# Performance work log

Hardware: AMD Instinct MI355X
Metric: run time of the kernel (lower is better)

Reference implementation:

```python
import jax, jax.numpy as jnp
import numpy as np

DIM = 1024
DEPTH = 7
PAR = 8
N_NODES = 2 ** (DEPTH + 1) - 1  # 255
WIDTH = PAR * N_NODES  # 2040


def setup_inputs() -> dict:
    key = jax.random.key(0)
    k1, k2, k3, k4 = jax.random.split(key, 4)
    init_k = float(np.sqrt(1.0 / DIM))
    init_k2 = float(np.sqrt(1.0 / ((DEPTH + 1) * PAR)))
    oldx = jax.random.normal(k1, (4, 2048, DIM), dtype=jnp.float32)
    W_in = jax.random.uniform(k2, (WIDTH, DIM), jnp.float32, -init_k, init_k)
    b_in = jax.random.uniform(k3, (WIDTH,), jnp.float32, -init_k, init_k)
    W_out = jax.random.uniform(k4, (DIM, WIDTH), jnp.float32, -init_k2, init_k2)
    return {"oldx": oldx, "W_in": W_in, "b_in": b_in, "W_out": W_out}


def reference(oldx, W_in, b_in, W_out):
    x = oldx.reshape(-1, DIM)                      # [B, dim]
    B = x.shape[0]
    logits = x @ W_in.T + b_in                     # [B, width] dense GEMM over ALL nodes
    decisions = (logits > 0).astype(jnp.int32).reshape(B, PAR, N_NODES)
    acts = jax.nn.silu(logits).reshape(B, PAR, N_NODES)

    # Tree traversal: mark root, then descend DEPTH levels by each node's sign bit.
    current = jnp.zeros((B, PAR), dtype=jnp.int32)
    dmap = jax.nn.one_hot(current, N_NODES, dtype=acts.dtype)  # root node marked
    for d in range(DEPTH):
        cur_platform = 2 ** d - 1
        next_platform = 2 ** (d + 1) - 1
        moves = jnp.take_along_axis(decisions, current[..., None], axis=2)[..., 0]
        current = (current - cur_platform) * 2 + moves + next_platform
        dmap = dmap + jax.nn.one_hot(current, N_NODES, dtype=acts.dtype)

    masked = acts * jax.lax.stop_gradient(dmap)    # only depth+1 nodes per tree survive
    out = masked.reshape(B, WIDTH) @ W_out.T       # [B, dim]
    return out.reshape(oldx.shape)
```

## Files before the change

kernel.cpp:

```cpp
#include <hip/hip_runtime.h>
#include <math.h>

#define DIM 1024
#define DEPTH 7
#define PAR 8
#define N_NODES 255
#define WIDTH 2040
#define MARGIN 0.03f

#define REPLANE(p) ((((p) & 1) << 3) | ((((p) >> 1) & 1) << 4) | ((((p) >> 2) & 1) << 5))

typedef float  float2v  __attribute__((ext_vector_type(2)));
typedef _Float16 half2v __attribute__((ext_vector_type(2)));

__device__ __forceinline__ unsigned short f32_to_bf16(float f) {
    unsigned int u = __float_as_uint(f);
    u += 0x7fffu + ((u >> 16) & 1u);
    return (unsigned short)(u >> 16);
}
__device__ __forceinline__ float bf_lo(unsigned int u) { return __uint_as_float(u << 16); }
__device__ __forceinline__ float bf_hi(unsigned int u) { return __uint_as_float(u & 0xffff0000u); }

__device__ __forceinline__ half2v as_h2(unsigned int u) {
    union { unsigned int u; half2v h; } c; c.u = u; return c.h;
}
__device__ __forceinline__ unsigned int pack_h2(float a, float b) {
    union { half2v h; unsigned int u; } c;
    c.h = (half2v){(_Float16)a, (_Float16)b};
    return c.u;
}

__device__ __forceinline__ float dot2h(unsigned int a, unsigned int b, float c) {
#if __has_builtin(__builtin_amdgcn_fdot2)
    return __builtin_amdgcn_fdot2(as_h2(a), as_h2(b), c, false);
#else
    half2v ha = as_h2(a), hb = as_h2(b);
    c = fmaf((float)ha.x, (float)hb.x, c);
    return fmaf((float)ha.y, (float)hb.y, c);
#endif
}

__device__ __forceinline__ float foldK(float a, float b, int K) {
    const bool hi = (threadIdx.x & (unsigned)K) != 0;
    const float keep = hi ? b : a;
    const float send = hi ? a : b;
    return keep + __shfl_xor(send, K, 64);
}

__global__ __launch_bounds__(256) void convert_f16_kernel(
    const float* __restrict__ src, unsigned int* __restrict__ dst, int n4)
{
    int i = (int)(blockIdx.x * blockDim.x + threadIdx.x);
    if (i < n4) {
        float4 v = ((const float4*)src)[i];
        uint2 pk;
        pk.x = pack_h2(v.x, v.y);
        pk.y = pack_h2(v.z, v.w);
        ((uint2*)dst)[i] = pk;
    }
}

__global__ __launch_bounds__(256) void transpose_bf16_kernel(
    const float* __restrict__ W_out, unsigned short* __restrict__ WoT)
{
    __shared__ float tile[64][65];
    const int w0 = blockIdx.x * 64;
    const int d0 = blockIdx.y * 64;
    const int tid = (int)threadIdx.x;
    const int sub = tid & 15;
    const int grp = tid >> 4;

    #pragma unroll
    for (int pass = 0; pass < 4; ++pass) {
        const int dl = pass * 16 + grp;
        const int wl = sub * 4;
        const int w = w0 + wl;
        const int d = d0 + dl;
        float4 v = make_float4(0.f, 0.f, 0.f, 0.f);
        if (w + 3 < WIDTH) {
            v = *(const float4*)(W_out + (size_t)d * WIDTH + w);
        } else {
            float t0 = (w + 0 < WIDTH) ? W_out[(size_t)d * WIDTH + w + 0] : 0.f;
            float t1 = (w + 1 < WIDTH) ? W_out[(size_t)d * WIDTH + w + 1] : 0.f;
            float t2 = (w + 2 < WIDTH) ? W_out[(size_t)d * WIDTH + w + 2] : 0.f;
            float t3 = (w + 3 < WIDTH) ? W_out[(size_t)d * WIDTH + w + 3] : 0.f;
            v = make_float4(t0, t1, t2, t3);
        }
        tile[dl][wl + 0] = v.x; tile[dl][wl + 1] = v.y;
        tile[dl][wl + 2] = v.z; tile[dl][wl + 3] = v.w;
    }
    __syncthreads();
    #pragma unroll
    for (int pass = 0; pass < 4; ++pass) {
        const int wl = pass * 16 + grp;
        const int dl = sub * 4;
        const int w = w0 + wl;
        if (w < WIDTH) {
            unsigned int b0 = f32_to_bf16(tile[dl + 0][wl]);
            unsigned int b1 = f32_to_bf16(tile[dl + 1][wl]);
            unsigned int b2 = f32_to_bf16(tile[dl + 2][wl]);
            unsigned int b3 = f32_to_bf16(tile[dl + 3][wl]);
            uint2 pk;
            pk.x = b0 | (b1 << 16);
            pk.y = b2 | (b3 << 16);
            *(uint2*)(WoT + (size_t)w * DIM + d0 + dl) = pk;
        }
    }
}

__global__ __launch_bounds__(256, 2) void fff_f16_kernel(
    const float* __restrict__ x,
    const float* __restrict__ W_in,
    const float* __restrict__ b_in,
    const unsigned int* __restrict__ Wh,
    const unsigned short* __restrict__ WoT,
    float* __restrict__ out,
    int B)
{
    const int wave = (int)((blockIdx.x * blockDim.x + threadIdx.x) >> 6);
    const int lane = (int)(threadIdx.x & 63);
    if (wave >= B) return;

    const float* xr = x + (size_t)wave * DIM;
    unsigned int xp[8];
    {
        float4 a0 = *(const float4*)(xr + lane * 8 + 0);
        float4 a1 = *(const float4*)(xr + lane * 8 + 4);
        float4 a2 = *(const float4*)(xr + 512 + lane * 8 + 0);
        float4 a3 = *(const float4*)(xr + 512 + lane * 8 + 4);
        xp[0] = pack_h2(a0.x, a0.y);
        xp[1] = pack_h2(a0.z, a0.w);
        xp[2] = pack_h2(a1.x, a1.y);
        xp[3] = pack_h2(a1.z, a1.w);
        xp[4] = pack_h2(a2.x, a2.y);
        xp[5] = pack_h2(a2.z, a2.w);
        xp[6] = pack_h2(a3.x, a3.y);
        xp[7] = pack_h2(a3.z, a3.w);
    }

    float2v acc2[8];
    #pragma unroll
    for (int i = 0; i < 8; ++i) acc2[i] = (float2v){0.f, 0.f};

    unsigned long long nodes = 0ULL;
    const int myp = ((lane >> 3) & 1) | (((lane >> 4) & 1) << 1) | (((lane >> 5) & 1) << 2);

    #pragma unroll 1
    for (int d = 0; d <= DEPTH; ++d) {
        int gidx[PAR];
        float partial[PAR];
        uint4 wo0[PAR], wo1[PAR];

        #pragma unroll
        for (int p = 0; p < PAR; ++p) {
            const int np = (int)((nodes >> (8 * p)) & 0xffULL);
            gidx[p] = p * N_NODES + np;
        }
        #pragma unroll
        for (int p = 0; p < PAR; ++p) {
            const unsigned short* wo = WoT + (size_t)gidx[p] * DIM;
            wo0[p] = *(const uint4*)(wo + lane * 8);
            wo1[p] = *(const uint4*)(wo + 512 + lane * 8);
        }
        #pragma unroll
        for (int p = 0; p < PAR; ++p) {
            const unsigned int* wr = Wh + (size_t)gidx[p] * (DIM / 2);
            const uint4 u0 = *(const uint4*)(wr + lane * 4);
            const uint4 u1 = *(const uint4*)(wr + 256 + lane * 4);
            float s = 0.f;
            s = dot2h(xp[0], u0.x, s);
            s = dot2h(xp[1], u0.y, s);
            s = dot2h(xp[2], u0.z, s);
            s = dot2h(xp[3], u0.w, s);
            s = dot2h(xp[4], u1.x, s);
            s = dot2h(xp[5], u1.y, s);
            s = dot2h(xp[6], u1.z, s);
            s = dot2h(xp[7], u1.w, s);
            partial[p] = s;
        }

        const float c01 = foldK(partial[0], partial[1], 8);
        const float c23 = foldK(partial[2], partial[3], 8);
        const float c45 = foldK(partial[4], partial[5], 8);
        const float c67 = foldK(partial[6], partial[7], 8);
        const float d0f = foldK(c01, c23, 16);
        const float d1f = foldK(c45, c67, 16);
        float e = foldK(d0f, d1f, 32);
        e += __shfl_xor(e, 1, 64);
        e += __shfl_xor(e, 2, 64);
        e += __shfl_xor(e, 4, 64);

        const int ga = (lane & 8) ? gidx[1] : gidx[0];
        const int gb = (lane & 8) ? gidx[3] : gidx[2];
        const int gc = (lane & 8) ? gidx[5] : gidx[4];
        const int gd = (lane & 8) ? gidx[7] : gidx[6];
        const int ge = (lane & 16) ? gb : ga;
        const int gf = (lane & 16) ? gd : gc;
        const int gmine = (lane & 32) ? gf : ge;
        float my = e + b_in[gmine];

        if (d < DEPTH) {
            const unsigned long long bal = __ballot(fabsf(my) < MARGIN);
            unsigned rm = 0;
            #pragma unroll
            for (int p = 0; p < PAR; ++p)
                rm |= ((unsigned)((bal >> REPLANE(p)) & 1ULL)) << p;
            if (rm) {
                const float4 fa = *(const float4*)(xr + lane * 8 + 0);
                const float4 fb = *(const float4*)(xr + lane * 8 + 4);
                const float4 fc = *(const float4*)(xr + 512 + lane * 8 + 0);
                const float4 fd = *(const float4*)(xr + 512 + lane * 8 + 4);
                while (rm) {
                    const int p = __builtin_ctz(rm); rm &= (rm - 1u);
                    const int np = (int)((nodes >> (8 * p)) & 0xffULL);
                    const int gi = p * N_NODES + np;
                    const float* wr = W_in + (size_t)gi * DIM;
                    const float4 wa = *(const float4*)(wr + lane * 8 + 0);
                    const float4 wb = *(const float4*)(wr + lane * 8 + 4);
                    const float4 wc = *(const float4*)(wr + 512 + lane * 8 + 0);
                    const float4 wd = *(const float4*)(wr + 512 + lane * 8 + 4);
                    float s = 0.f;
                    s = fmaf(fa.x, wa.x, s); s = fmaf(fa.y, wa.y, s);
                    s = fmaf(fa.z, wa.z, s); s = fmaf(fa.w, wa.w, s);
                    s = fmaf(fb.x, wb.x, s); s = fmaf(fb.y, wb.y, s);
                    s = fmaf(fb.z, wb.z, s); s = fmaf(fb.w, wb.w, s);
                    s = fmaf(fc.x, wc.x, s); s = fmaf(fc.y, wc.y, s);
                    s = fmaf(fc.z, wc.z, s); s = fmaf(fc.w, wc.w, s);
                    s = fmaf(fd.x, wd.x, s); s = fmaf(fd.y, wd.y, s);
                    s = fmaf(fd.z, wd.z, s); s = fmaf(fd.w, wd.w, s);
                    #pragma unroll
                    for (int off = 32; off >= 1; off >>= 1)
                        s += __shfl_xor(s, off, 64);
                    const float lf = s + b_in[gi];
                    my = (myp == p) ? lf : my;
                }
            }
        }

        const float act_mine = my / (1.0f + __expf(-my));
        const unsigned long long pos = __ballot(my > 0.0f);

        float act[PAR];
        #pragma unroll
        for (int p = 0; p < PAR; ++p)
            act[p] = __shfl(act_mine, REPLANE(p), 64);

        #pragma unroll
        for (int p = 0; p < PAR; ++p) {
            const uint4 u0 = wo0[p];
            const uint4 u1 = wo1[p];
            const float2v a2 = (float2v){act[p], act[p]};
            acc2[0] += a2 * (float2v){bf_lo(u0.x), bf_hi(u0.x)};
            acc2[1] += a2 * (float2v){bf_lo(u0.y), bf_hi(u0.y)};
            acc2[2] += a2 * (float2v){bf_lo(u0.z), bf_hi(u0.z)};
            acc2[3] += a2 * (float2v){bf_lo(u0.w), bf_hi(u0.w)};
            acc2[4] += a2 * (float2v){bf_lo(u1.x), bf_hi(u1.x)};
            acc2[5] += a2 * (float2v){bf_lo(u1.y), bf_hi(u1.y)};
            acc2[6] += a2 * (float2v){bf_lo(u1.z), bf_hi(u1.z)};
            acc2[7] += a2 * (float2v){bf_lo(u1.w), bf_hi(u1.w)};

            if (d < DEPTH) {
                const int np = (int)((nodes >> (8 * p)) & 0xffULL);
                const unsigned long long nn = (unsigned long long)
                    (2 * np + 1 + (int)((pos >> REPLANE(p)) & 1ULL));
                nodes = (nodes & ~(0xffULL << (8 * p))) | (nn << (8 * p));
            }
        }
    }

    float* orow = out + (size_t)wave * DIM;
    *(float4*)(orow + lane * 8 + 0) =
        make_float4(acc2[0].x, acc2[0].y, acc2[1].x, acc2[1].y);
    *(float4*)(orow + lane * 8 + 4) =
        make_float4(acc2[2].x, acc2[2].y, acc2[3].x, acc2[3].y);
    *(float4*)(orow + 512 + lane * 8 + 0) =
        make_float4(acc2[4].x, acc2[4].y, acc2[5].x, acc2[5].y);
    *(float4*)(orow + 512 + lane * 8 + 4) =
        make_float4(acc2[6].x, acc2[6].y, acc2[7].x, acc2[7].y);
}

__global__ __launch_bounds__(256) void fff_fallback_kernel(
    const float* __restrict__ x, const float* __restrict__ W_in,
    const float* __restrict__ b_in, const float* __restrict__ W_out,
    float* __restrict__ out, int B)
{
    const int wave = (int)((blockIdx.x * blockDim.x + threadIdx.x) >> 6);
    const int lane = (int)(threadIdx.x & 63);
    if (wave >= B) return;

    const float* xr = x + (size_t)wave * DIM;
    float4 x4[4];
    x4[0] = *(const float4*)(xr + lane * 8 + 0);
    x4[1] = *(const float4*)(xr + lane * 8 + 4);
    x4[2] = *(const float4*)(xr + 512 + lane * 8 + 0);
    x4[3] = *(const float4*)(xr + 512 + lane * 8 + 4);

    float acc[16];
    #pragma unroll
    for (int i = 0; i < 16; ++i) acc[i] = 0.f;
    int node[PAR];
    #pragma unroll
    for (int p = 0; p < PAR; ++p) node[p] = 0;

    for (int d = 0; d <= DEPTH; ++d) {
        #pragma unroll
        for (int p = 0; p < PAR; ++p) {
            const int gidx = p * N_NODES + node[p];
            const float* wr = W_in + (size_t)gidx * DIM;
            const float4 wa = *(const float4*)(wr + lane * 8 + 0);
            const float4 wb = *(const float4*)(wr + lane * 8 + 4);
            const float4 wc = *(const float4*)(wr + 512 + lane * 8 + 0);
            const float4 wd = *(const float4*)(wr + 512 + lane * 8 + 4);
            float s = 0.f;
            s = fmaf(x4[0].x, wa.x, s); s = fmaf(x4[0].y, wa.y, s);
            s = fmaf(x4[0].z, wa.z, s); s = fmaf(x4[0].w, wa.w, s);
            s = fmaf(x4[1].x, wb.x, s); s = fmaf(x4[1].y, wb.y, s);
            s = fmaf(x4[1].z, wb.z, s); s = fmaf(x4[1].w, wb.w, s);
            s = fmaf(x4[2].x, wc.x, s); s = fmaf(x4[2].y, wc.y, s);
            s = fmaf(x4[2].z, wc.z, s); s = fmaf(x4[2].w, wc.w, s);
            s = fmaf(x4[3].x, wd.x, s); s = fmaf(x4[3].y, wd.y, s);
            s = fmaf(x4[3].z, wd.z, s); s = fmaf(x4[3].w, wd.w, s);
            #pragma unroll
            for (int off = 32; off >= 1; off >>= 1)
                s += __shfl_xor(s, off, 64);
            const float logit = s + b_in[gidx];
            const float act = logit / (1.0f + __expf(-logit));
            #pragma unroll
            for (int k = 0; k < 2; ++k) {
                #pragma unroll
                for (int j = 0; j < 8; ++j) {
                    const int e = k * 512 + lane * 8 + j;
                    acc[k * 8 + j] = fmaf(act, W_out[(size_t)e * WIDTH + gidx], acc[k * 8 + j]);
                }
            }
            node[p] = 2 * node[p] + 1 + ((logit > 0.0f) ? 1 : 0);
        }
    }

    float* orow = out + (size_t)wave * DIM;
    *(float4*)(orow + lane * 8 + 0)       = make_float4(acc[0],  acc[1],  acc[2],  acc[3]);
    *(float4*)(orow + lane * 8 + 4)       = make_float4(acc[4],  acc[5],  acc[6],  acc[7]);
    *(float4*)(orow + 512 + lane * 8 + 0) = make_float4(acc[8],  acc[9],  acc[10], acc[11]);
    *(float4*)(orow + 512 + lane * 8 + 4) = make_float4(acc[12], acc[13], acc[14], acc[15]);
}

extern "C" void kernel_launch(void* const* d_in, const int* in_sizes, int n_in,
                              void* d_out, int out_size, void* d_ws, size_t ws_size,
                              hipStream_t stream) {
    const float* oldx  = (const float*)d_in[0];
    const float* W_in  = (const float*)d_in[1];
    const float* b_in  = (const float*)d_in[2];
    const float* W_out = (const float*)d_in[3];
    float* out = (float*)d_out;

    const int B = in_sizes[0] / DIM;

    const size_t half = (size_t)WIDTH * DIM * sizeof(unsigned short);
    const bool use_lp = (ws_size >= 2 * half) && (d_ws != nullptr);

    const int blocks = (B + 3) / 4;

    if (use_lp) {
        unsigned short* WoT = (unsigned short*)d_ws;
        unsigned int*   Wh  = (unsigned int*)((char*)d_ws + half);
        dim3 tg((WIDTH + 63) / 64, DIM / 64);
        transpose_bf16_kernel<<<tg, 256, 0, stream>>>(W_out, WoT);
        const int n4 = WIDTH * DIM / 4;
        convert_f16_kernel<<<(n4 + 255) / 256, 256, 0, stream>>>(W_in, Wh, n4);
        fff_f16_kernel<<<blocks, 256, 0, stream>>>(oldx, W_in, b_in, Wh, WoT, out, B);
    } else {
        fff_fallback_kernel<<<blocks, 256, 0, stream>>>(oldx, W_in, b_in, W_out, out, B);
    }
}
```

Measured before the change: 188.7 us.

## Process two rows per wavefront and defer W_out loads until after activation

Each wavefront now handles two batch rows at once, interleaving their gather loads, dot products, reductions and accumulations so that more independent memory requests are in flight per wave. The W_out row loads move from before the logit computation to just before the accumulation, which shortens register live ranges. The launch-bounds occupancy hint is dropped and the grid is halved. Register pressure roughly doubles, which may reduce occupancy or cause spills, and the rows within a wave can diverge on the rare fp32 recompute path.

```diff
diff --git a/kernel.cpp b/kernel.cpp
--- a/kernel.cpp
+++ b/kernel.cpp
@@ -108,7 +108,7 @@
     }
 }
 
-__global__ __launch_bounds__(256, 2) void fff_f16_kernel(
+__global__ __launch_bounds__(256) void fff_f16x2_kernel(
     const float* __restrict__ x,
     const float* __restrict__ W_in,
     const float* __restrict__ b_in,
@@ -117,166 +117,216 @@
     float* __restrict__ out,
     int B)
 {
-    const int wave = (int)((blockIdx.x * blockDim.x + threadIdx.x) >> 6);
-    const int lane = (int)(threadIdx.x & 63);
-    if (wave >= B) return;
-
-    const float* xr = x + (size_t)wave * DIM;
-    unsigned int xp[8];
+    const int wpair = (int)((blockIdx.x * blockDim.x + threadIdx.x) >> 6);
+    const int lane  = (int)(threadIdx.x & 63);
+    const int r0 = 2 * wpair;
+    const int r1 = 2 * wpair + 1;
+    if (r0 >= B) return;
+    const bool has1 = (r1 < B);
+
+    const float* xr0 = x + (size_t)r0 * DIM;
+    const float* xr1 = x + (size_t)(has1 ? r1 : r0) * DIM;
+
+    unsigned int xp0[8], xp1[8];
     {
-        float4 a0 = *(const float4*)(xr + lane * 8 + 0);
-        float4 a1 = *(const float4*)(xr + lane * 8 + 4);
-        float4 a2 = *(const float4*)(xr + 512 + lane * 8 + 0);
-        float4 a3 = *(const float4*)(xr + 512 + lane * 8 + 4);
-        xp[0] = pack_h2(a0.x, a0.y);
-        xp[1] = pack_h2(a0.z, a0.w);
-        xp[2] = pack_h2(a1.x, a1.y);
-        xp[3] = pack_h2(a1.z, a1.w);
-        xp[4] = pack_h2(a2.x, a2.y);
-        xp[5] = pack_h2(a2.z, a2.w);
-        xp[6] = pack_h2(a3.x, a3.y);
-        xp[7] = pack_h2(a3.z, a3.w);
-    }
-
-    float2v acc2[8];
+        float4 a0 = *(const float4*)(xr0 + lane * 8 + 0);
+        float4 a1 = *(const float4*)(xr0 + lane * 8 + 4);
+        float4 a2 = *(const float4*)(xr0 + 512 + lane * 8 + 0);
+        float4 a3 = *(const float4*)(xr0 + 512 + lane * 8 + 4);
+        float4 b0 = *(const float4*)(xr1 + lane * 8 + 0);
+        float4 b1 = *(const float4*)(xr1 + lane * 8 + 4);
+        float4 b2 = *(const float4*)(xr1 + 512 + lane * 8 + 0);
+        float4 b3 = *(const float4*)(xr1 + 512 + lane * 8 + 4);
+        xp0[0] = pack_h2(a0.x, a0.y); xp0[1] = pack_h2(a0.z, a0.w);
+        xp0[2] = pack_h2(a1.x, a1.y); xp0[3] = pack_h2(a1.z, a1.w);
+        xp0[4] = pack_h2(a2.x, a2.y); xp0[5] = pack_h2(a2.z, a2.w);
+        xp0[6] = pack_h2(a3.x, a3.y); xp0[7] = pack_h2(a3.z, a3.w);
+        xp1[0] = pack_h2(b0.x, b0.y); xp1[1] = pack_h2(b0.z, b0.w);
+        xp1[2] = pack_h2(b1.x, b1.y); xp1[3] = pack_h2(b1.z, b1.w);
+        xp1[4] = pack_h2(b2.x, b2.y); xp1[5] = pack_h2(b2.z, b2.w);
+        xp1[6] = pack_h2(b3.x, b3.y); xp1[7] = pack_h2(b3.z, b3.w);
+    }
+
+    float2v acc0[8], acc1[8];
     #pragma unroll
-    for (int i = 0; i < 8; ++i) acc2[i] = (float2v){0.f, 0.f};
-
-    unsigned long long nodes = 0ULL;
+    for (int i = 0; i < 8; ++i) { acc0[i] = (float2v){0.f, 0.f}; acc1[i] = (float2v){0.f, 0.f}; }
+
+    unsigned long long nodes0 = 0ULL, nodes1 = 0ULL;
     const int myp = ((lane >> 3) & 1) | (((lane >> 4) & 1) << 1) | (((lane >> 5) & 1) << 2);
 
     #pragma unroll 1
     for (int d = 0; d <= DEPTH; ++d) {
-        int gidx[PAR];
-        float partial[PAR];
-        uint4 wo0[PAR], wo1[PAR];
+        int g0[PAR], g1[PAR];
+        float pa0[PAR], pa1[PAR];
 
         #pragma unroll
         for (int p = 0; p < PAR; ++p) {
-            const int np = (int)((nodes >> (8 * p)) & 0xffULL);
-            gidx[p] = p * N_NODES + np;
-        }
+            g0[p] = p * N_NODES + (int)((nodes0 >> (8 * p)) & 0xffULL);
+            g1[p] = p * N_NODES + (int)((nodes1 >> (8 * p)) & 0xffULL);
+        }
+
         #pragma unroll
         for (int p = 0; p < PAR; ++p) {
-            const unsigned short* wo = WoT + (size_t)gidx[p] * DIM;
-            wo0[p] = *(const uint4*)(wo + lane * 8);
-            wo1[p] = *(const uint4*)(wo + 512 + lane * 8);
-        }
+            const unsigned int* wr0 = Wh + (size_t)g0[p] * (DIM / 2);
+            const unsigned int* wr1 = Wh + (size_t)g1[p] * (DIM / 2);
+            const uint4 u0 = *(const uint4*)(wr0 + lane * 4);
+            const uint4 u1 = *(const uint4*)(wr0 + 256 + lane * 4);
+            const uint4 v0 = *(const uint4*)(wr1 + lane * 4);
+            const uint4 v1 = *(const uint4*)(wr1 + 256 + lane * 4);
+            float s0 = 0.f, s1 = 0.f;
+            s0 = dot2h(xp0[0], u0.x, s0);  s1 = dot2h(xp1[0], v0.x, s1);
+            s0 = dot2h(xp0[1], u0.y, s0);  s1 = dot2h(xp1[1], v0.y, s1);
+            s0 = dot2h(xp0[2], u0.z, s0);  s1 = dot2h(xp1[2], v0.z, s1);
+            s0 = dot2h(xp0[3], u0.w, s0);  s1 = dot2h(xp1[3], v0.w, s1);
+            s0 = dot2h(xp0[4], u1.x, s0);  s1 = dot2h(xp1[4], v1.x, s1);
+            s0 = dot2h(xp0[5], u1.y, s0);  s1 = dot2h(xp1[5], v1.y, s1);
+            s0 = dot2h(xp0[6], u1.z, s0);  s1 = dot2h(xp1[6], v1.z, s1);
+            s0 = dot2h(xp0[7], u1.w, s0);  s1 = dot2h(xp1[7], v1.w, s1);
+            pa0[p] = s0; pa1[p] = s1;
+        }
+
+        const float c01a = foldK(pa0[0], pa0[1], 8),  c01b = foldK(pa1[0], pa1[1], 8);
+        const float c23a = foldK(pa0[2], pa0[3], 8),  c23b = foldK(pa1[2], pa1[3], 8);
+        const float c45a = foldK(pa0[4], pa0[5], 8),  c45b = foldK(pa1[4], pa1[5], 8);
+        const float c67a = foldK(pa0[6], pa0[7], 8),  c67b = foldK(pa1[6], pa1[7], 8);
+        const float d0a = foldK(c01a, c23a, 16),      d0b = foldK(c01b, c23b, 16);
+        const float d1a = foldK(c45a, c67a, 16),      d1b = foldK(c45b, c67b, 16);
+        float e0 = foldK(d0a, d1a, 32);
+        float e1 = foldK(d0b, d1b, 32);
+        e0 += __shfl_xor(e0, 1, 64);  e1 += __shfl_xor(e1, 1, 64);
+        e0 += __shfl_xor(e0, 2, 64);  e1 += __shfl_xor(e1, 2, 64);
+        e0 += __shfl_xor(e0, 4, 64);  e1 += __shfl_xor(e1, 4, 64);
+
+        int gm0, gm1;
+        {
+            const int a0 = (lane & 8) ? g0[1] : g0[0];
+            const int a1 = (lane & 8) ? g0[3] : g0[2];
+            const int a2 = (lane & 8) ? g0[5] : g0[4];
+            const int a3 = (lane & 8) ? g0[7] : g0[6];
+            const int b0 = (lane & 16) ? a1 : a0;
+            const int b1 = (lane & 16) ? a3 : a2;
+            gm0 = (lane & 32) ? b1 : b0;
+            const int c0 = (lane & 8) ? g1[1] : g1[0];
+            const int c1 = (lane & 8) ? g1[3] : g1[2];
+            const int c2 = (lane & 8) ? g1[5] : g1[4];
+            const int c3 = (lane & 8) ? g1[7] : g1[6];
+            const int e0i = (lane & 16) ? c1 : c0;
+            const int e1i = (lane & 16) ? c3 : c2;
+            gm1 = (lane & 32) ? e1i : e0i;
+        }
+        float my0 = e0 + b_in[gm0];
+        float my1 = e1 + b_in[gm1];
+
+        if (d < DEPTH) {
+            const unsigned long long bal0 = __ballot(fabsf(my0) < MARGIN);
+            const unsigned long long bal1 = has1 ? __ballot(fabsf(my1) < MARGIN) : 0ULL;
+            unsigned rm0 = 0, rm1 = 0;
+            #pragma unroll
+            for (int p = 0; p < PAR; ++p) {
+                rm0 |= ((unsigned)((bal0 >> REPLANE(p)) & 1ULL)) << p;
+                rm1 |= ((unsigned)((bal1 >> REPLANE(p)) & 1ULL)) << p;
+            }
+            if (rm0 | rm1) {
+                #pragma unroll 1
+                for (int r = 0; r < 2; ++r) {
+                    unsigned rm = r ? rm1 : rm0;
+                    if (!rm) continue;
+                    const float* xrr = r ? xr1 : xr0;
+                    const float4 fa = *(const float4*)(xrr + lane * 8 + 0);
+                    const float4 fb = *(const float4*)(xrr + lane * 8 + 4);
+                    const float4 fc = *(const float4*)(xrr + 512 + lane * 8 + 0);
+                    const float4 fd = *(const float4*)(xrr + 512 + lane * 8 + 4);
+                    while (rm) {
+                        const int p = __builtin_ctz(rm); rm &= (rm - 1u);
+                        const int gi = r ? g1[p] : g0[p];
+                        const float* wr = W_in + (size_t)gi * DIM;
+                        const float4 wa = *(const float4*)(wr + lane * 8 + 0);
+                        const float4 wb = *(const float4*)(wr + lane * 8 + 4);
+                        const float4 wc = *(const float4*)(wr + 512 + lane * 8 + 0);
+                        const float4 wd = *(const float4*)(wr + 512 + lane * 8 + 4);
+                        float s = 0.f;
+                        s = fmaf(fa.x, wa.x, s); s = fmaf(fa.y, wa.y, s);
+                        s = fmaf(fa.z, wa.z, s); s = fmaf(fa.w, wa.w, s);
+                        s = fmaf(fb.x, wb.x, s); s = fmaf(fb.y, wb.y, s);
+                        s = fmaf(fb.z, wb.z, s); s = fmaf(fb.w, wb.w, s);
+                        s = fmaf(fc.x, wc.x, s); s = fmaf(fc.y, wc.y, s);
+                        s = fmaf(fc.z, wc.z, s); s = fmaf(fc.w, wc.w, s);
+                        s = fmaf(fd.x, wd.x, s); s = fmaf(fd.y, wd.y, s);
+                        s = fmaf(fd.z, wd.z, s); s = fmaf(fd.w, wd.w, s);
+                        #pragma unroll
+                        for (int off = 32; off >= 1; off >>= 1)
+                            s += __shfl_xor(s, off, 64);
+                        const float lf = s + b_in[gi];
+                        if (myp == p) { if (r) my1 = lf; else my0 = lf; }
+                    }
+                }
+            }
+        }
+
+        const float am0 = my0 / (1.0f + __expf(-my0));
+        const float am1 = my1 / (1.0f + __expf(-my1));
+        const unsigned long long pos0 = __ballot(my0 > 0.0f);
+        const unsigned long long pos1 = __ballot(my1 > 0.0f);
+
+        float act0[PAR], act1[PAR];
         #pragma unroll
         for (int p = 0; p < PAR; ++p) {
-            const unsigned int* wr = Wh + (size_t)gidx[p] * (DIM / 2);
-            const uint4 u0 = *(const uint4*)(wr + lane * 4);
-            const uint4 u1 = *(const uint4*)(wr + 256 + lane * 4);
-            float s = 0.f;
-            s = dot2h(xp[0], u0.x, s);
-            s = dot2h(xp[1], u0.y, s);
-            s = dot2h(xp[2], u0.z, s);
-            s = dot2h(xp[3], u0.w, s);
-            s = dot2h(xp[4], u1.x, s);
-            s = dot2h(xp[5], u1.y, s);
-            s = dot2h(xp[6], u1.z, s);
-            s = dot2h(xp[7], u1.w, s);
-            partial[p] = s;
-        }
-
-        const float c01 = foldK(partial[0], partial[1], 8);
-        const float c23 = foldK(partial[2], partial[3], 8);
-        const float c45 = foldK(partial[4], partial[5], 8);
-        const float c67 = foldK(partial[6], partial[7], 8);
-        const float d0f = foldK(c01, c23, 16);
-        const float d1f = foldK(c45, c67, 16);
-        float e = foldK(d0f, d1f, 32);
-        e += __shfl_xor(e, 1, 64);
-        e += __shfl_xor(e, 2, 64);
-        e += __shfl_xor(e, 4, 64);
-
-        const int ga = (lane & 8) ? gidx[1] : gidx[0];
-        const int gb = (lane & 8) ? gidx[3] : gidx[2];
-        const int gc = (lane & 8) ? gidx[5] : gidx[4];
-        const int gd = (lane & 8) ? gidx[7] : gidx[6];
-        const int ge = (lane & 16) ? gb : ga;
-        const int gf = (lane & 16) ? gd : gc;
-        const int gmine = (lane & 32) ? gf : ge;
-        float my = e + b_in[gmine];
-
-        if (d < DEPTH) {
-            const unsigned long long bal = __ballot(fabsf(my) < MARGIN);
-            unsigned rm = 0;
-            #pragma unroll
-            for (int p = 0; p < PAR; ++p)
-                rm |= ((unsigned)((bal >> REPLANE(p)) & 1ULL)) << p;
-            if (rm) {
-                const float4 fa = *(const float4*)(xr + lane * 8 + 0);
-                const float4 fb = *(const float4*)(xr + lane * 8 + 4);
-                const float4 fc = *(const float4*)(xr + 512 + lane * 8 + 0);
-                const float4 fd = *(const float4*)(xr + 512 + lane * 8 + 4);
-                while (rm) {
-                    const int p = __builtin_ctz(rm); rm &= (rm - 1u);
-                    const int np = (int)((nodes >> (8 * p)) & 0xffULL);
-                    const int gi = p * N_NODES + np;
-                    const float* wr = W_in + (size_t)gi * DIM;
-                    const float4 wa = *(const float4*)(wr + lane * 8 + 0);
-                    const float4 wb = *(const float4*)(wr + lane * 8 + 4);
-                    const float4 wc = *(const float4*)(wr + 512 + lane * 8 + 0);
-                    const float4 wd = *(const float4*)(wr + 512 + lane * 8 + 4);
-                    float s = 0.f;
-                    s = fmaf(fa.x, wa.x, s); s = fmaf(fa.y, wa.y, s);
-                    s = fmaf(fa.z, wa.z, s); s = fmaf(fa.w, wa.w, s);
-                    s = fmaf(fb.x, wb.x, s); s = fmaf(fb.y, wb.y, s);
-                    s = fmaf(fb.z, wb.z, s); s = fmaf(fb.w, wb.w, s);
-                    s = fmaf(fc.x, wc.x, s); s = fmaf(fc.y, wc.y, s);
-                    s = fmaf(fc.z, wc.z, s); s = fmaf(fc.w, wc.w, s);
-                    s = fmaf(fd.x, wd.x, s); s = fmaf(fd.y, wd.y, s);
-                    s = fmaf(fd.z, wd.z, s); s = fmaf(fd.w, wd.w, s);
-                    #pragma unroll
-                    for (int off = 32; off >= 1; off >>= 1)
-                        s += __shfl_xor(s, off, 64);
-                    const float lf = s + b_in[gi];
-                    my = (myp == p) ? lf : my;
-                }
-            }
-        }
-
-        const float act_mine = my / (1.0f + __expf(-my));
-        const unsigned long long pos = __ballot(my > 0.0f);
-
-        float act[PAR];
-        #pragma unroll
-        for (int p = 0; p < PAR; ++p)
-            act[p] = __shfl(act_mine, REPLANE(p), 64);
+            act0[p] = __shfl(am0, REPLANE(p), 64);
+            act1[p] = __shfl(am1, REPLANE(p), 64);
+        }
 
         #pragma unroll
         for (int p = 0; p < PAR; ++p) {
-            const uint4 u0 = wo0[p];
-            const uint4 u1 = wo1[p];
-            const float2v a2 = (float2v){act[p], act[p]};
-            acc2[0] += a2 * (float2v){bf_lo(u0.x), bf_hi(u0.x)};
-            acc2[1] += a2 * (float2v){bf_lo(u0.y), bf_hi(u0.y)};
-            acc2[2] += a2 * (float2v){bf_lo(u0.z), bf_hi(u0.z)};
-            acc2[3] += a2 * (float2v){bf_lo(u0.w), bf_hi(u0.w)};
-            acc2[4] += a2 * (float2v){bf_lo(u1.x), bf_hi(u1.x)};
-            acc2[5] += a2 * (float2v){bf_lo(u1.y), bf_hi(u1.y)};
-            acc2[6] += a2 * (float2v){bf_lo(u1.z), bf_hi(u1.z)};
-            acc2[7] += a2 * (float2v){bf_lo(u1.w), bf_hi(u1.w)};
+            const unsigned short* wo0 = WoT + (size_t)g0[p] * DIM;
+            const unsigned short* wo1 = WoT + (size_t)g1[p] * DIM;
+            const uint4 u0 = *(const uint4*)(wo0 + lane * 8);
+            const uint4 u1 = *(const uint4*)(wo0 + 512 + lane * 8);
+            const uint4 v0 = *(const uint4*)(wo1 + lane * 8);
+            const uint4 v1 = *(const uint4*)(wo1 + 512 + lane * 8);
+            const float2v A0 = (float2v){act0[p], act0[p]};
+            const float2v A1 = (float2v){act1[p], act1[p]};
+            acc0[0] += A0 * (float2v){bf_lo(u0.x), bf_hi(u0.x)};
+            acc0[1] += A0 * (float2v){bf_lo(u0.y), bf_hi(u0.y)};
+            acc0[2] += A0 * (float2v){bf_lo(u0.z), bf_hi(u0.z)};
+            acc0[3] += A0 * (float2v){bf_lo(u0.w), bf_hi(u0.w)};
+            acc0[4] += A0 * (float2v){bf_lo(u1.x), bf_hi(u1.x)};
+            acc0[5] += A0 * (float2v){bf_lo(u1.y), bf_hi(u1.y)};
+            acc0[6] += A0 * (float2v){bf_lo(u1.z), bf_hi(u1.z)};
+            acc0[7] += A0 * (float2v){bf_lo(u1.w), bf_hi(u1.w)};
+            acc1[0] += A1 * (float2v){bf_lo(v0.x), bf_hi(v0.x)};
+            acc1[1] += A1 * (float2v){bf_lo(v0.y), bf_hi(v0.y)};
+            acc1[2] += A1 * (float2v){bf_lo(v0.z), bf_hi(v0.z)};
+            acc1[3] += A1 * (float2v){bf_lo(v0.w), bf_hi(v0.w)};
+            acc1[4] += A1 * (float2v){bf_lo(v1.x), bf_hi(v1.x)};
+            acc1[5] += A1 * (float2v){bf_lo(v1.y), bf_hi(v1.y)};
+            acc1[6] += A1 * (float2v){bf_lo(v1.z), bf_hi(v1.z)};
+            acc1[7] += A1 * (float2v){bf_lo(v1.w), bf_hi(v1.w)};
 
             if (d < DEPTH) {
-                const int np = (int)((nodes >> (8 * p)) & 0xffULL);
-                const unsigned long long nn = (unsigned long long)
-                    (2 * np + 1 + (int)((pos >> REPLANE(p)) & 1ULL));
-                nodes = (nodes & ~(0xffULL << (8 * p))) | (nn << (8 * p));
+                const int np0 = (int)((nodes0 >> (8 * p)) & 0xffULL);
+                const int np1 = (int)((nodes1 >> (8 * p)) & 0xffULL);
+                const unsigned long long nn0 = (unsigned long long)
+                    (2 * np0 + 1 + (int)((pos0 >> REPLANE(p)) & 1ULL));
+                const unsigned long long nn1 = (unsigned long long)
+                    (2 * np1 + 1 + (int)((pos1 >> REPLANE(p)) & 1ULL));
+                nodes0 = (nodes0 & ~(0xffULL << (8 * p))) | (nn0 << (8 * p));
+                nodes1 = (nodes1 & ~(0xffULL << (8 * p))) | (nn1 << (8 * p));
             }
         }
     }
 
-    float* orow = out + (size_t)wave * DIM;
-    *(float4*)(orow + lane * 8 + 0) =
-        make_float4(acc2[0].x, acc2[0].y, acc2[1].x, acc2[1].y);
-    *(float4*)(orow + lane * 8 + 4) =
-        make_float4(acc2[2].x, acc2[2].y, acc2[3].x, acc2[3].y);
-    *(float4*)(orow + 512 + lane * 8 + 0) =
-        make_float4(acc2[4].x, acc2[4].y, acc2[5].x, acc2[5].y);
-    *(float4*)(orow + 512 + lane * 8 + 4) =
-        make_float4(acc2[6].x, acc2[6].y, acc2[7].x, acc2[7].y);
+    float* o0 = out + (size_t)r0 * DIM;
+    *(float4*)(o0 + lane * 8 + 0)       = make_float4(acc0[0].x, acc0[0].y, acc0[1].x, acc0[1].y);
+    *(float4*)(o0 + lane * 8 + 4)       = make_float4(acc0[2].x, acc0[2].y, acc0[3].x, acc0[3].y);
+    *(float4*)(o0 + 512 + lane * 8 + 0) = make_float4(acc0[4].x, acc0[4].y, acc0[5].x, acc0[5].y);
+    *(float4*)(o0 + 512 + lane * 8 + 4) = make_float4(acc0[6].x, acc0[6].y, acc0[7].x, acc0[7].y);
+    if (has1) {
+        float* o1 = out + (size_t)r1 * DIM;
+        *(float4*)(o1 + lane * 8 + 0)       = make_float4(acc1[0].x, acc1[0].y, acc1[1].x, acc1[1].y);
+        *(float4*)(o1 + lane * 8 + 4)       = make_float4(acc1[2].x, acc1[2].y, acc1[3].x, acc1[3].y);
+        *(float4*)(o1 + 512 + lane * 8 + 0) = make_float4(acc1[4].x, acc1[4].y, acc1[5].x, acc1[5].y);
+        *(float4*)(o1 + 512 + lane * 8 + 4) = make_float4(acc1[6].x, acc1[6].y, acc1[7].x, acc1[7].y);
+    }
 }
 
 __global__ __launch_bounds__(256) void fff_fallback_kernel(
@@ -358,8 +408,6 @@
     const size_t half = (size_t)WIDTH * DIM * sizeof(unsigned short);
     const bool use_lp = (ws_size >= 2 * half) && (d_ws != nullptr);
 
-    const int blocks = (B + 3) / 4;
-
     if (use_lp) {
         unsigned short* WoT = (unsigned short*)d_ws;
         unsigned int*   Wh  = (unsigned int*)((char*)d_ws + half);
@@ -367,8 +415,11 @@
         transpose_bf16_kernel<<<tg, 256, 0, stream>>>(W_out, WoT);
         const int n4 = WIDTH * DIM / 4;
         convert_f16_kernel<<<(n4 + 255) / 256, 256, 0, stream>>>(W_in, Wh, n4);
-        fff_f16_kernel<<<blocks, 256, 0, stream>>>(oldx, W_in, b_in, Wh, WoT, out, B);
+        const int npairs = (B + 1) / 2;
+        const int blocks = (npairs * 64 + 255) / 256;
+        fff_f16x2_kernel<<<blocks, 256, 0, stream>>>(oldx, W_in, b_in, Wh, WoT, out, B);
     } else {
+        const int blocks = (B + 3) / 4;
         fff_fallback_kernel<<<blocks, 256, 0, stream>>>(oldx, W_in, b_in, W_out, out, B);
     }
 }
```

Result: slower. 226.2 us (+19.9%).
